# Kernel tuning notes

Hardware: AMD Instinct MI355X
Metric: run time of the kernel (lower is better)

The kernel has to match this reference:

```python
import jax, jax.numpy as jnp
import numpy as np

N_NODES = 50000
N_EDGES = 800000
D_IN, D_HID, D_OUT = 128, 64, 64


def gcn_conv(x, W, b, src, dst, num_nodes):
    """PyG-style GCNConv: add self-loops, symmetric norm, aggregate at target.
    src/dst already include self-loops. x: [N, Din], W: [Din, Dout]."""
    xw = x @ W  # transform first (Din -> Dout), like PyG
    ew = jnp.ones(src.shape[0], dtype=x.dtype)
    deg = jax.ops.segment_sum(ew, dst, num_segments=num_nodes)
    dis = jnp.where(deg > 0, jax.lax.rsqrt(deg), 0.0)  # deg^{-1/2}
    norm = dis[src] * ew * dis[dst]  # [E+N]
    msgs = norm[:, None] * xw[src]  # gather source features
    out = jax.ops.segment_sum(msgs, dst, num_segments=num_nodes)
    return out + b


def setup_inputs() -> dict:
    key = jax.random.key(0)
    ks = jax.random.split(key, 8)
    x = jax.random.normal(ks[0], (N_NODES, D_IN), dtype=jnp.float32)
    edge_index = jax.random.randint(ks[1], (2, N_EDGES), 0, N_NODES, dtype=jnp.int64)
    W1 = jax.random.normal(ks[2], (D_IN, D_HID), dtype=jnp.float32) * (1.0 / np.sqrt(D_IN))
    b1 = jnp.zeros((D_HID,), dtype=jnp.float32)
    W2 = jax.random.normal(ks[3], (D_HID, D_HID), dtype=jnp.float32) * (1.0 / np.sqrt(D_HID))
    b2 = jnp.zeros((D_HID,), dtype=jnp.float32)
    W3 = jax.random.normal(ks[4], (D_HID, D_OUT), dtype=jnp.float32) * (1.0 / np.sqrt(D_HID))
    b3 = jnp.zeros((D_OUT,), dtype=jnp.float32)
    return {"x": x, "edge_index": edge_index, "W1": W1, "b1": b1,
            "W2": W2, "b2": b2, "W3": W3, "b3": b3}


def reference(x, edge_index, W1, b1, W2, b2, W3, b3):
    # Add self-loops once (shared by all layers), as PyG GCNConv does per layer.
    loop = jnp.arange(N_NODES, dtype=edge_index.dtype)
    src = jnp.concatenate([edge_index[0], loop])
    dst = jnp.concatenate([edge_index[1], loop])
    # Layer 1 + ReLU (dropout is identity in eval mode)
    h = gcn_conv(x, W1, b1, src, dst, N_NODES)
    h = jax.nn.relu(h)
    # Layer 2 + ReLU
    h = gcn_conv(h, W2, b2, src, dst, N_NODES)
    h = jax.nn.relu(h)
    # Layer 3 (no activation)
    out = gcn_conv(h, W3, b3, src, dst, N_NODES)
    return out
```

## Files before the change

### kernel.cpp

```cpp
#include <hip/hip_runtime.h>
#include <hip/hip_fp16.h>

#define N_NODES 50000
#define N_PAD   50048
#define N_EDGES 800000
#define E_TOT   (N_EDGES + N_NODES)
#define D_IN    128
#define D_HID   64

#define NB         196
#define EB_CHUNK   4096
#define BIN_BLOCKS 196

typedef __bf16 bf16x8 __attribute__((ext_vector_type(8)));
typedef float  f32x4  __attribute__((ext_vector_type(4)));


template <int K>
__device__ __forceinline__ void pack_w(const float* __restrict__ W,
                                       __bf16* __restrict__ Bh, __bf16* __restrict__ Bl, int i) {
  constexpr int KS = K / 32;
  int j = i & 7, lane = (i >> 3) & 63, rest = i >> 9;
  int ct = rest / KS, ks = rest - ct * KS;
  int k = ks * 32 + ((lane >> 4) << 3) + j;
  int c = ct * 16 + (lane & 15);
  float v = W[k * 64 + c];
  __bf16 hb = (__bf16)v;
  Bh[i] = hb;
  Bl[i] = (__bf16)(v - (float)hb);
}


__global__ __launch_bounds__(256) void k_binc_sw(const int* __restrict__ dst,
                                                 unsigned* __restrict__ blkcnt,
                                                 const float* __restrict__ W1,
                                                 const float* __restrict__ W2,
                                                 const float* __restrict__ W3,
                                                 __bf16* __restrict__ Wh1, __bf16* __restrict__ Wl1,
                                                 __bf16* __restrict__ Wh2, __bf16* __restrict__ Wl2,
                                                 __bf16* __restrict__ Wh3, __bf16* __restrict__ Wl3) {
  __shared__ unsigned lh[256];
  int blk = blockIdx.x, t = threadIdx.x;
  if (blk < BIN_BLOCKS) {
    lh[t] = 0;
    __syncthreads();
    int base = blk * EB_CHUNK;
    int endv = min(base + EB_CHUNK, N_EDGES);
    for (int e = base + t; e < endv; e += 256)
      atomicAdd(&lh[((unsigned)dst[e]) >> 8], 1u);
    __syncthreads();
    blkcnt[blk * 256 + t] = lh[t];
  } else {
    int b = blk - BIN_BLOCKS;
    if (b < 32)      pack_w<D_IN >(W1, Wh1, Wl1, b * 256 + t);
    else if (b < 48) pack_w<D_HID>(W2, Wh2, Wl2, (b - 32) * 256 + t);
    else             pack_w<D_HID>(W3, Wh3, Wl3, (b - 48) * 256 + t);
  }
}


__global__ __launch_bounds__(256) void k_bscan(const unsigned* __restrict__ blkcnt,
                                               unsigned* __restrict__ blkoff,
                                               unsigned* __restrict__ bucket_cnt,
                                               unsigned* __restrict__ bucket_ebase,
                                               unsigned* __restrict__ bucket_cbase,
                                               unsigned* __restrict__ rowptr) {
  __shared__ unsigned se[256], sc[256];
  int t = threadIdx.x;
  unsigned run = 0;
  for (int b = 0; b < BIN_BLOCKS; b++) {
    unsigned c = blkcnt[b * 256 + t];
    blkoff[b * 256 + t] = run;
    run += c;
  }
  bucket_cnt[t] = run;
  unsigned cnt   = (t < NB) ? run : 0u;
  unsigned nodes = (t < NB) ? (unsigned)min(256, N_NODES - t * 256) : 0u;
  unsigned ctot  = cnt + nodes;
  se[t] = cnt; sc[t] = ctot;
  __syncthreads();
  for (int off = 1; off < 256; off <<= 1) {
    unsigned a = (t >= off) ? se[t - off] : 0u;
    unsigned b = (t >= off) ? sc[t - off] : 0u;
    __syncthreads();
    se[t] += a; sc[t] += b;
    __syncthreads();
  }
  if (t < NB) {
    bucket_ebase[t] = se[t] - cnt;
    bucket_cbase[t] = sc[t] - ctot;
  }
  if (t == 0) rowptr[N_NODES] = E_TOT;
}


__global__ __launch_bounds__(256) void k_bins(const int* __restrict__ src,
                                              const int* __restrict__ dst,
                                              const unsigned* __restrict__ bucket_ebase,
                                              const unsigned* __restrict__ blkoff,
                                              unsigned* __restrict__ temp) {
  __shared__ unsigned lcur[256];
  int blk = blockIdx.x, t = threadIdx.x;
  lcur[t] = bucket_ebase[t] + blkoff[blk * 256 + t];
  __syncthreads();
  int base = blk * EB_CHUNK;
  int endv = min(base + EB_CHUNK, N_EDGES);
  for (int e = base + t; e < endv; e += 256) {
    unsigned d = (unsigned)dst[e];
    unsigned pos = atomicAdd(&lcur[d >> 8], 1u);
    temp[pos] = (unsigned)src[e] | ((d & 255u) << 16);
  }
}


template <int K, bool FIRST>
__device__ __forceinline__ void gemm_body(int bid,
                                          const float* __restrict__ Xf,
                                          const __bf16* __restrict__ Ah,
                                          const __bf16* __restrict__ Al,
                                          const __bf16* __restrict__ Bh,
                                          const __bf16* __restrict__ Bl,
                                          __half* __restrict__ Y) {
  constexpr int KS = K / 32;
  const int tid  = threadIdx.x;
  const int wave = tid >> 6;
  const int lane = tid & 63;
  const int row0 = bid * 64 + wave * 16;
  const int row_a = FIRST ? min(row0 + (lane & 15), N_NODES - 1)
                          : row0 + (lane & 15);
  const int q8 = (lane >> 4) << 3;

  f32x4 acc[4];
#pragma unroll
  for (int ct = 0; ct < 4; ct++) acc[ct] = (f32x4){0.f, 0.f, 0.f, 0.f};

#pragma unroll
  for (int ks = 0; ks < KS; ks++) {
    bf16x8 ah, al;
    if (FIRST) {
      const float4* xr4 = reinterpret_cast<const float4*>(Xf + (size_t)row_a * K);
      float4 f0 = xr4[ks * 8 + (q8 >> 2) + 0];
      float4 f1 = xr4[ks * 8 + (q8 >> 2) + 1];
#pragma unroll
      for (int j = 0; j < 4; j++) {
        float a0 = (&f0.x)[j], a1 = (&f1.x)[j];
        __bf16 h0 = (__bf16)a0, h1 = (__bf16)a1;
        ah[j] = h0;     al[j] = (__bf16)(a0 - (float)h0);
        ah[4 + j] = h1; al[4 + j] = (__bf16)(a1 - (float)h1);
      }
    } else {
      size_t abase = (size_t)row_a * K + q8 + ks * 32;
      ah = *reinterpret_cast<const bf16x8*>(Ah + abase);
      al = *reinterpret_cast<const bf16x8*>(Al + abase);
    }
#pragma unroll
    for (int ct = 0; ct < 4; ct++) {
      bf16x8 bh = *reinterpret_cast<const bf16x8*>(Bh + (size_t)((ct * KS + ks) * 64 + lane) * 8);
      bf16x8 bl = *reinterpret_cast<const bf16x8*>(Bl + (size_t)((ct * KS + ks) * 64 + lane) * 8);
      acc[ct] = __builtin_amdgcn_mfma_f32_16x16x32_bf16(ah, bh, acc[ct], 0, 0, 0);
      acc[ct] = __builtin_amdgcn_mfma_f32_16x16x32_bf16(ah, bl, acc[ct], 0, 0, 0);
      acc[ct] = __builtin_amdgcn_mfma_f32_16x16x32_bf16(al, bh, acc[ct], 0, 0, 0);
    }
  }

  const int rbase = row0 + ((lane >> 4) << 2);
  const int c     = lane & 15;
#pragma unroll
  for (int ct = 0; ct < 4; ct++)
#pragma unroll
    for (int r = 0; r < 4; r++) {
      int row = rbase + r;
      if (row < N_NODES)
        Y[(size_t)row * 64 + ct * 16 + c] = __float2half_rn(acc[ct][r]);
    }
}


__global__ __launch_bounds__(256) void k_csr_gemm1(const unsigned* __restrict__ temp,
                                                   const unsigned* __restrict__ bucket_ebase,
                                                   const unsigned* __restrict__ bucket_cnt,
                                                   const unsigned* __restrict__ bucket_cbase,
                                                   unsigned* __restrict__ rowptr,
                                                   float* __restrict__ dis,
                                                   unsigned* __restrict__ csr,
                                                   const float* __restrict__ x,
                                                   const __bf16* __restrict__ Wh1,
                                                   const __bf16* __restrict__ Wl1,
                                                   __half* __restrict__ xw) {
  __shared__ unsigned hist[256], sscan[256], lfill[256];
  if (blockIdx.x >= NB) {
    gemm_body<D_IN, true>(blockIdx.x - NB, x, nullptr, nullptr, Wh1, Wl1, xw);
    return;
  }
  int b = blockIdx.x, t = threadIdx.x;
  unsigned ebase = bucket_ebase[b], ecnt = bucket_cnt[b], cbase = bucket_cbase[b];
  int nodes = min(256, N_NODES - b * 256);
  hist[t] = 0;
  __syncthreads();
  for (unsigned i = t; i < ecnt; i += 256)
    atomicAdd(&hist[(temp[ebase + i] >> 16) & 255u], 1u);
  __syncthreads();
  unsigned deg = (t < nodes) ? hist[t] + 1u : 0u;
  sscan[t] = deg;
  __syncthreads();
  for (int off = 1; off < 256; off <<= 1) {
    unsigned v = (t >= off) ? sscan[t - off] : 0u;
    __syncthreads();
    sscan[t] += v;
    __syncthreads();
  }
  unsigned excl = sscan[t] - deg;
  if (t < nodes) {
    int node = b * 256 + t;
    rowptr[node] = cbase + excl;
    dis[node] = rsqrtf((float)deg);
    csr[cbase + excl] = (unsigned)node;
  }
  lfill[t] = excl + 1u;
  __syncthreads();
  for (unsigned i = t; i < ecnt; i += 256) {
    unsigned v = temp[ebase + i];
    unsigned d = (v >> 16) & 255u;
    unsigned pos = atomicAdd(&lfill[d], 1u);
    csr[cbase + pos] = v & 0xFFFFu;
  }
}


__global__ __launch_bounds__(256) void k_gemm23(const __bf16* __restrict__ Ah,
                                                const __bf16* __restrict__ Al,
                                                const __bf16* __restrict__ Bh,
                                                const __bf16* __restrict__ Bl,
                                                __half* __restrict__ Y) {
  gemm_body<D_HID, false>(blockIdx.x, nullptr, Ah, Al, Bh, Bl, Y);
}


template <int MODE>
__global__ __launch_bounds__(256) void k_agg(const float4* __restrict__ XW4,
                                             const unsigned* __restrict__ rowptr,
                                             const unsigned* __restrict__ csr,
                                             const float* __restrict__ dis,
                                             const float4* __restrict__ bias4,
                                             __bf16* __restrict__ hh,
                                             __bf16* __restrict__ hl,
                                             float4* __restrict__ OUT4) {
  int node = (int)((blockIdx.x * blockDim.x + threadIdx.x) >> 6);
  int lane = threadIdx.x & 63;
  if (node >= N_NODES) return;
  const int sub = lane & 7;
  const int grp = lane >> 3;

  const float disd = dis[node];
  unsigned beg = rowptr[node], end = rowptr[node + 1];
  float acc0[8] = {0,0,0,0,0,0,0,0};
  float acc1[8] = {0,0,0,0,0,0,0,0};

  for (unsigned j = beg; j < end; j += 64) {
    int nj = (int)min(64u, end - j);
    unsigned s = 0u; float nrm = 0.f;
    if (lane < nj) {
      s = csr[j + lane];
      nrm = dis[s] * disd;
    }
    for (int k = 0; k < nj; k += 16) {
      int e0 = k + grp;
      unsigned s0 = (unsigned)__shfl((int)s, e0);
      float    n0 = __shfl(nrm, e0);
      float4 v0 = XW4[(size_t)s0 * 8 + sub];
      const __half2* h0 = reinterpret_cast<const __half2*>(&v0);
#pragma unroll
      for (int q = 0; q < 4; q++) {
        float2 f = __half22float2(h0[q]);
        acc0[2*q]   += n0 * f.x;
        acc0[2*q+1] += n0 * f.y;
      }
      if (k + 8 < nj) {
        int e1 = k + grp + 8;
        unsigned s1 = (unsigned)__shfl((int)s, e1);
        float    n1 = __shfl(nrm, e1);
        float4 v1 = XW4[(size_t)s1 * 8 + sub];
        const __half2* h1 = reinterpret_cast<const __half2*>(&v1);
#pragma unroll
        for (int q = 0; q < 4; q++) {
          float2 f = __half22float2(h1[q]);
          acc1[2*q]   += n1 * f.x;
          acc1[2*q+1] += n1 * f.y;
        }
      }
    }
  }

  float acc[8];
#pragma unroll
  for (int i = 0; i < 8; i++) acc[i] = acc0[i] + acc1[i];
#pragma unroll
  for (int i = 0; i < 8; i++) {
    acc[i] += __shfl_xor(acc[i], 8);
    acc[i] += __shfl_xor(acc[i], 16);
    acc[i] += __shfl_xor(acc[i], 32);
  }

  if (grp == 0) {
    float4 ba = bias4[sub * 2], bb = bias4[sub * 2 + 1];
    acc[0] += ba.x; acc[1] += ba.y; acc[2] += ba.z; acc[3] += ba.w;
    acc[4] += bb.x; acc[5] += bb.y; acc[6] += bb.z; acc[7] += bb.w;
    if (MODE == 0) {
      bf16x8 hv, lv;
#pragma unroll
      for (int i = 0; i < 8; i++) {
        float f = fmaxf(acc[i], 0.f);
        __bf16 hb = (__bf16)f;
        hv[i] = hb;
        lv[i] = (__bf16)(f - (float)hb);
      }
      *reinterpret_cast<bf16x8*>(&hh[(size_t)node * 64 + sub * 8]) = hv;
      *reinterpret_cast<bf16x8*>(&hl[(size_t)node * 64 + sub * 8]) = lv;
    } else {
      float4 o0 = {acc[0], acc[1], acc[2], acc[3]};
      float4 o1 = {acc[4], acc[5], acc[6], acc[7]};
      OUT4[(size_t)node * 16 + sub * 2]     = o0;
      OUT4[(size_t)node * 16 + sub * 2 + 1] = o1;
    }
  }
}


extern "C" void kernel_launch(void* const* d_in, const int* in_sizes, int n_in,
                              void* d_out, int out_size, void* d_ws, size_t ws_size,
                              hipStream_t stream) {
  const float* x    = (const float*)d_in[0];
  const int*   eidx = (const int*)d_in[1];
  const float* W1   = (const float*)d_in[2];
  const float* b1   = (const float*)d_in[3];
  const float* W2   = (const float*)d_in[4];
  const float* b2   = (const float*)d_in[5];
  const float* W3   = (const float*)d_in[6];
  const float* b3   = (const float*)d_in[7];
  float* out = (float*)d_out;

  const int* e_src = eidx;
  const int* e_dst = eidx + N_EDGES;

  size_t off = 0;
  auto alloc = [&](size_t bytes) -> void* {
    void* p = (char*)d_ws + off;
    off += (bytes + 255) & ~(size_t)255;
    return p;
  };
  unsigned* rowptr  = (unsigned*)alloc((size_t)(N_NODES + 1) * 4);
  float*    dis     = (float*)alloc((size_t)N_NODES * 4);
  unsigned* csr     = (unsigned*)alloc((size_t)E_TOT * 4);
  unsigned* temp    = (unsigned*)alloc((size_t)N_EDGES * 4);
  unsigned* blkcnt  = (unsigned*)alloc((size_t)BIN_BLOCKS * 256 * 4);
  unsigned* blkoff  = (unsigned*)alloc((size_t)BIN_BLOCKS * 256 * 4);
  unsigned* bcnt    = (unsigned*)alloc(256 * 4);
  unsigned* bebase  = (unsigned*)alloc(256 * 4);
  unsigned* bcbase  = (unsigned*)alloc(256 * 4);
  __half*   xw      = (__half*)alloc((size_t)N_PAD * 64 * 2);
  __bf16*   hhA     = (__bf16*)alloc((size_t)N_PAD * 64 * 2);
  __bf16*   hlA     = (__bf16*)alloc((size_t)N_PAD * 64 * 2);
  __bf16*   hhB     = (__bf16*)alloc((size_t)N_PAD * 64 * 2);
  __bf16*   hlB     = (__bf16*)alloc((size_t)N_PAD * 64 * 2);
  __bf16*   Wh1     = (__bf16*)alloc((size_t)D_IN * 64 * 2);
  __bf16*   Wl1     = (__bf16*)alloc((size_t)D_IN * 64 * 2);
  __bf16*   Wh2     = (__bf16*)alloc((size_t)D_HID * 64 * 2);
  __bf16*   Wl2     = (__bf16*)alloc((size_t)D_HID * 64 * 2);
  __bf16*   Wh3     = (__bf16*)alloc((size_t)D_HID * 64 * 2);
  __bf16*   Wl3     = (__bf16*)alloc((size_t)D_HID * 64 * 2);

  const int gemm_grid = N_PAD / 64;
  const int agg_grid  = (N_NODES * 64 + 255) / 256;

  k_binc_sw<<<BIN_BLOCKS + 64, 256, 0, stream>>>(e_dst, blkcnt, W1, W2, W3,
                                                 Wh1, Wl1, Wh2, Wl2, Wh3, Wl3);
  k_bscan<<<1, 256, 0, stream>>>(blkcnt, blkoff, bcnt, bebase, bcbase, rowptr);
  k_bins<<<BIN_BLOCKS, 256, 0, stream>>>(e_src, e_dst, bebase, blkoff, temp);
  k_csr_gemm1<<<NB + gemm_grid, 256, 0, stream>>>(temp, bebase, bcnt, bcbase,
                                                  rowptr, dis, csr, x, Wh1, Wl1, xw);
  k_agg<0><<<agg_grid, 256, 0, stream>>>((const float4*)xw, rowptr, csr, dis,
                                         (const float4*)b1, hhA, hlA, nullptr);
  k_gemm23<<<gemm_grid, 256, 0, stream>>>(hhA, hlA, Wh2, Wl2, xw);
  k_agg<0><<<agg_grid, 256, 0, stream>>>((const float4*)xw, rowptr, csr, dis,
                                         (const float4*)b2, hhB, hlB, nullptr);
  k_gemm23<<<gemm_grid, 256, 0, stream>>>(hhB, hlB, Wh3, Wl3, xw);
  k_agg<1><<<agg_grid, 256, 0, stream>>>((const float4*)xw, rowptr, csr, dis,
                                         (const float4*)b3, nullptr, nullptr, (float4*)out);
}
```

Before: 139.7 us.

## Split aggregation feature halves across two waves and store CSR indices as 16-bit

Each node's aggregation is now handled by two wavefronts, one per 32-column half of the feature row. Each wavefront uses 4 lanes per edge, so it processes 16 edges per step instead of 8, which gives more memory-level parallelism and more waves to hide gather latency. The CSR neighbour indices shrink from 32-bit to 16-bit, which is valid because node ids are below 65536, and this halves index traffic. The cost is that every wave now reads rowptr, csr and dis twice, and it does extra shuffle reductions.

```diff
diff --git a/kernel.cpp b/kernel.cpp
--- a/kernel.cpp
+++ b/kernel.cpp
@@ -182,7 +182,7 @@
                                                    const unsigned* __restrict__ bucket_cbase,
                                                    unsigned* __restrict__ rowptr,
                                                    float* __restrict__ dis,
-                                                   unsigned* __restrict__ csr,
+                                                   unsigned short* __restrict__ csr,
                                                    const float* __restrict__ x,
                                                    const __bf16* __restrict__ Wh1,
                                                    const __bf16* __restrict__ Wl1,
@@ -214,7 +214,7 @@
     int node = b * 256 + t;
     rowptr[node] = cbase + excl;
     dis[node] = rsqrtf((float)deg);
-    csr[cbase + excl] = (unsigned)node;
+    csr[cbase + excl] = (unsigned short)node;
   }
   lfill[t] = excl + 1u;
   __syncthreads();
@@ -222,7 +222,7 @@
     unsigned v = temp[ebase + i];
     unsigned d = (v >> 16) & 255u;
     unsigned pos = atomicAdd(&lfill[d], 1u);
-    csr[cbase + pos] = v & 0xFFFFu;
+    csr[cbase + pos] = (unsigned short)(v & 0xFFFFu);
   }
 }
 
@@ -239,17 +239,18 @@
 template <int MODE>
 __global__ __launch_bounds__(256) void k_agg(const float4* __restrict__ XW4,
                                              const unsigned* __restrict__ rowptr,
-                                             const unsigned* __restrict__ csr,
+                                             const unsigned short* __restrict__ csr,
                                              const float* __restrict__ dis,
                                              const float4* __restrict__ bias4,
                                              __bf16* __restrict__ hh,
                                              __bf16* __restrict__ hl,
                                              float4* __restrict__ OUT4) {
-  int node = (int)((blockIdx.x * blockDim.x + threadIdx.x) >> 6);
+  int wid  = (int)((blockIdx.x * blockDim.x + threadIdx.x) >> 6);
   int lane = threadIdx.x & 63;
-  if (node >= N_NODES) return;
-  const int sub = lane & 7;
-  const int grp = lane >> 3;
+  const int half = (wid >= N_NODES) ? 1 : 0;
+  const int node = wid - half * N_NODES;
+  const int sub = lane & 3;
+  const int grp = lane >> 2;
 
   const float disd = dis[node];
   unsigned beg = rowptr[node], end = rowptr[node + 1];
@@ -263,11 +264,11 @@
       s = csr[j + lane];
       nrm = dis[s] * disd;
     }
-    for (int k = 0; k < nj; k += 16) {
+    for (int k = 0; k < nj; k += 32) {
       int e0 = k + grp;
       unsigned s0 = (unsigned)__shfl((int)s, e0);
       float    n0 = __shfl(nrm, e0);
-      float4 v0 = XW4[(size_t)s0 * 8 + sub];
+      float4 v0 = XW4[(size_t)s0 * 8 + half * 4 + sub];
       const __half2* h0 = reinterpret_cast<const __half2*>(&v0);
 #pragma unroll
       for (int q = 0; q < 4; q++) {
@@ -275,11 +276,11 @@
         acc0[2*q]   += n0 * f.x;
         acc0[2*q+1] += n0 * f.y;
       }
-      if (k + 8 < nj) {
-        int e1 = k + grp + 8;
+      if (k + 16 < nj) {
+        int e1 = k + grp + 16;
         unsigned s1 = (unsigned)__shfl((int)s, e1);
         float    n1 = __shfl(nrm, e1);
-        float4 v1 = XW4[(size_t)s1 * 8 + sub];
+        float4 v1 = XW4[(size_t)s1 * 8 + half * 4 + sub];
         const __half2* h1 = reinterpret_cast<const __half2*>(&v1);
 #pragma unroll
         for (int q = 0; q < 4; q++) {
@@ -296,13 +297,14 @@
   for (int i = 0; i < 8; i++) acc[i] = acc0[i] + acc1[i];
 #pragma unroll
   for (int i = 0; i < 8; i++) {
+    acc[i] += __shfl_xor(acc[i], 4);
     acc[i] += __shfl_xor(acc[i], 8);
     acc[i] += __shfl_xor(acc[i], 16);
     acc[i] += __shfl_xor(acc[i], 32);
   }
 
   if (grp == 0) {
-    float4 ba = bias4[sub * 2], bb = bias4[sub * 2 + 1];
+    float4 ba = bias4[half * 8 + sub * 2], bb = bias4[half * 8 + sub * 2 + 1];
     acc[0] += ba.x; acc[1] += ba.y; acc[2] += ba.z; acc[3] += ba.w;
     acc[4] += bb.x; acc[5] += bb.y; acc[6] += bb.z; acc[7] += bb.w;
     if (MODE == 0) {
@@ -314,13 +316,13 @@
         hv[i] = hb;
         lv[i] = (__bf16)(f - (float)hb);
       }
-      *reinterpret_cast<bf16x8*>(&hh[(size_t)node * 64 + sub * 8]) = hv;
-      *reinterpret_cast<bf16x8*>(&hl[(size_t)node * 64 + sub * 8]) = lv;
+      *reinterpret_cast<bf16x8*>(&hh[(size_t)node * 64 + half * 32 + sub * 8]) = hv;
+      *reinterpret_cast<bf16x8*>(&hl[(size_t)node * 64 + half * 32 + sub * 8]) = lv;
     } else {
       float4 o0 = {acc[0], acc[1], acc[2], acc[3]};
       float4 o1 = {acc[4], acc[5], acc[6], acc[7]};
-      OUT4[(size_t)node * 16 + sub * 2]     = o0;
-      OUT4[(size_t)node * 16 + sub * 2 + 1] = o1;
+      OUT4[(size_t)node * 16 + half * 8 + sub * 2]     = o0;
+      OUT4[(size_t)node * 16 + half * 8 + sub * 2 + 1] = o1;
     }
   }
 }
@@ -348,29 +350,29 @@
     off += (bytes + 255) & ~(size_t)255;
     return p;
   };
-  unsigned* rowptr  = (unsigned*)alloc((size_t)(N_NODES + 1) * 4);
-  float*    dis     = (float*)alloc((size_t)N_NODES * 4);
-  unsigned* csr     = (unsigned*)alloc((size_t)E_TOT * 4);
-  unsigned* temp    = (unsigned*)alloc((size_t)N_EDGES * 4);
-  unsigned* blkcnt  = (unsigned*)alloc((size_t)BIN_BLOCKS * 256 * 4);
-  unsigned* blkoff  = (unsigned*)alloc((size_t)BIN_BLOCKS * 256 * 4);
-  unsigned* bcnt    = (unsigned*)alloc(256 * 4);
-  unsigned* bebase  = (unsigned*)alloc(256 * 4);
-  unsigned* bcbase  = (unsigned*)alloc(256 * 4);
-  __half*   xw      = (__half*)alloc((size_t)N_PAD * 64 * 2);
-  __bf16*   hhA     = (__bf16*)alloc((size_t)N_PAD * 64 * 2);
-  __bf16*   hlA     = (__bf16*)alloc((size_t)N_PAD * 64 * 2);
-  __bf16*   hhB     = (__bf16*)alloc((size_t)N_PAD * 64 * 2);
-  __bf16*   hlB     = (__bf16*)alloc((size_t)N_PAD * 64 * 2);
-  __bf16*   Wh1     = (__bf16*)alloc((size_t)D_IN * 64 * 2);
-  __bf16*   Wl1     = (__bf16*)alloc((size_t)D_IN * 64 * 2);
-  __bf16*   Wh2     = (__bf16*)alloc((size_t)D_HID * 64 * 2);
-  __bf16*   Wl2     = (__bf16*)alloc((size_t)D_HID * 64 * 2);
-  __bf16*   Wh3     = (__bf16*)alloc((size_t)D_HID * 64 * 2);
-  __bf16*   Wl3     = (__bf16*)alloc((size_t)D_HID * 64 * 2);
+  unsigned*       rowptr = (unsigned*)alloc((size_t)(N_NODES + 1) * 4);
+  float*          dis    = (float*)alloc((size_t)N_NODES * 4);
+  unsigned short* csr    = (unsigned short*)alloc((size_t)E_TOT * 2);
+  unsigned*       temp   = (unsigned*)alloc((size_t)N_EDGES * 4);
+  unsigned*       blkcnt = (unsigned*)alloc((size_t)BIN_BLOCKS * 256 * 4);
+  unsigned*       blkoff = (unsigned*)alloc((size_t)BIN_BLOCKS * 256 * 4);
+  unsigned*       bcnt   = (unsigned*)alloc(256 * 4);
+  unsigned*       bebase = (unsigned*)alloc(256 * 4);
+  unsigned*       bcbase = (unsigned*)alloc(256 * 4);
+  __half*         xw     = (__half*)alloc((size_t)N_PAD * 64 * 2);
+  __bf16*         hhA    = (__bf16*)alloc((size_t)N_PAD * 64 * 2);
+  __bf16*         hlA    = (__bf16*)alloc((size_t)N_PAD * 64 * 2);
+  __bf16*         hhB    = (__bf16*)alloc((size_t)N_PAD * 64 * 2);
+  __bf16*         hlB    = (__bf16*)alloc((size_t)N_PAD * 64 * 2);
+  __bf16*         Wh1    = (__bf16*)alloc((size_t)D_IN * 64 * 2);
+  __bf16*         Wl1    = (__bf16*)alloc((size_t)D_IN * 64 * 2);
+  __bf16*         Wh2    = (__bf16*)alloc((size_t)D_HID * 64 * 2);
+  __bf16*         Wl2    = (__bf16*)alloc((size_t)D_HID * 64 * 2);
+  __bf16*         Wh3    = (__bf16*)alloc((size_t)D_HID * 64 * 2);
+  __bf16*         Wl3    = (__bf16*)alloc((size_t)D_HID * 64 * 2);
 
   const int gemm_grid = N_PAD / 64;
-  const int agg_grid  = (N_NODES * 64 + 255) / 256;
+  const int agg_grid  = (2 * N_NODES * 64) / 256;
 
   k_binc_sw<<<BIN_BLOCKS + 64, 256, 0, stream>>>(e_dst, blkcnt, W1, W2, W3,
                                                  Wh1, Wl1, Wh2, Wl2, Wh3, Wl3);
```

Result: slower. 192.4 us (+37.7%).
